# Kernel tuning notes

Hardware: AMD Instinct MI355X
Metric: run time of the kernel (lower is better)

## Reference

```python
import jax, jax.numpy as jnp
import numpy as np

FILTER = 3
STRIDE = 1


def setup_inputs() -> dict:
    key = jax.random.key(0)
    ks = jax.random.split(key, 6)
    B, P, N, d_in, d_ein, d_model = 16, 4, 4096, 128, 32, 128
    e_dim = FILTER * (FILTER - 1) * d_ein  # 192
    adj = jax.random.uniform(ks[0], (N, N), jnp.float32)
    features = jax.random.normal(ks[1], (B, N, d_in), jnp.float32)
    edge_features = jax.random.normal(ks[2], (B, N, e_dim), jnp.float32)
    mask = jax.random.uniform(ks[3], (P, N, 1), jnp.float32)
    W = jax.random.normal(ks[4], (FILTER * d_in + e_dim, d_model), jnp.float32) * 0.02
    b = jnp.zeros((d_model,), jnp.float32)
    return dict(adj=adj, features=features, edge_features=edge_features, mask=mask, W=W, b=b)


def reference(adj, features, edge_features, mask, W, b):
    Fs, S = FILTER, STRIDE
    B, N, d_in = features.shape
    # padding rule from _padding(): below_pad = filter - (N % stride or stride)
    below_pad = N % S
    below_pad = S if below_pad == 0 else below_pad
    below_pad = Fs - below_pad  # = 2 for stride=1, filter=3
    n_out = (N + below_pad - Fs) // S + 1  # = N

    feat_pad = jnp.pad(features, ((0, 0), (0, below_pad), (0, 0)))
    idx = jnp.arange(n_out)[:, None] * S + jnp.arange(Fs)[None, :]  # [n_out, F]
    win = feat_pad[:, idx, :]  # [B, n_out, F, d_in] (gather = torch unfold windows)
    jump = win.mean(axis=2)    # features.unfold(...).sum(-1)/filter -> [B, n_out, d_in]
    # torch unfold puts filter dim last: [B, n_out, d_in, F]; flatten(-2,-1) is d_in-major
    feat_flat = jnp.swapaxes(win, -1, -2).reshape(B, n_out, Fs * d_in)

    mask_pad = jnp.pad(mask, ((0, 0), (0, below_pad), (0, 0)))
    m = mask_pad[:, idx, :].max(axis=2)  # [P, n_out, 1]

    feat_cat = jnp.concatenate([feat_flat, edge_features], axis=-1)  # [B, n_out, 576]
    out = jax.nn.relu(feat_cat @ W + b)  # dropout is identity in eval
    res = out + jump  # residual (res=True)

    P = m.shape[0]
    d_model = out.shape[-1]
    out_m = (m * out.reshape(-1, P, n_out, d_model)).reshape(-1, n_out, d_model)
    res_m = (m * res.reshape(-1, P, n_out, d_model)).reshape(-1, n_out, d_model)
    return adj, res_m, out_m, m
```

## Files before the change

kernel.cpp:

```cpp
#include <hip/hip_runtime.h>
#include <hip/hip_bf16.h>

typedef __attribute__((ext_vector_type(8))) short short8;
typedef __attribute__((ext_vector_type(4))) float floatx4;

#define NN     4096
#define DIN    128
#define EDIM   192
#define DMODEL 128

__device__ __forceinline__ unsigned short f2bf(float f) {
    union { float f; unsigned int i; } x; x.f = f;
    unsigned int u = x.i;
    u += 0x7FFFu + ((u >> 16) & 1u);
    return (unsigned short)(u >> 16);
}

__device__ __forceinline__ unsigned int pk2(float lo, float hi) {
    union { __hip_bfloat162 v; unsigned int u; } cv;
    cv.v = __float22bfloat162_rn(make_float2(lo, hi));
    return cv.u;
}

__device__ __forceinline__ short8 cvt8(const float4 a, const float4 b) {
    union { short8 s; unsigned int u[4]; } r;
    r.u[0] = pk2(a.x, a.y);
    r.u[1] = pk2(a.z, a.w);
    r.u[2] = pk2(b.x, b.y);
    r.u[3] = pk2(b.z, b.w);
    return r.s;
}

__global__ void prep_w(const float* __restrict__ W, unsigned short* __restrict__ wf) {
    const int t = blockIdx.x * 256 + threadIdx.x;
    const int jj   = t & 7;
    const int lane = (t >> 3) & 63;
    const int ct   = (t >> 9) & 7;
    const int gs   = t >> 12;
    const int kt = gs * 32 + ((lane >> 4) << 3) + jj;
    const int korig = (kt < 384) ? ((kt & 127) * 3 + (kt >> 7)) : kt;
    const int n = ct * 16 + (lane & 15);
    wf[t] = f2bf(W[korig * DMODEL + n]);
}

__global__ __launch_bounds__(256, 2) void main_k(
    const float* __restrict__ feat,
    const float* __restrict__ edgef,
    const unsigned short* __restrict__ wfrag,
    const float* __restrict__ bias,
    const float* __restrict__ mask,
    const floatx4* __restrict__ adj4,
    floatx4* __restrict__ o_adj4,
    float* __restrict__ o_res,
    float* __restrict__ o_out,
    float* __restrict__ o_m)
{
    __shared__ float m3s[128];

    const int tid  = threadIdx.x;
    const int lane = tid & 63;
    const int wv   = tid >> 6;
    const int nn   = lane & 15;
    const int quad = lane >> 4;

    const int blk = blockIdx.x;
    const int b   = blk >> 5;
    const int i0  = (blk & 31) << 7;
    const int p   = b & 3;

    if (tid < 128) {
        const int i = i0 + tid;
        float v = mask[p * NN + i];
        if (i + 1 < NN) v = fmaxf(v, mask[p * NN + i + 1]);
        if (i + 2 < NN) v = fmaxf(v, mask[p * NN + i + 2]);
        m3s[tid] = v;
        if (b < 4) o_m[p * NN + i] = v;
    }
    __syncthreads();

    const float* fb = feat  + (size_t)b * NN * DIN;
    const float* eb = edgef + (size_t)b * NN * EDIM;

    const int rowb = i0 + wv * 32 + nn;

    floatx4 acc[2][8];
    #pragma unroll
    for (int rt = 0; rt < 2; ++rt)
        #pragma unroll
        for (int ct = 0; ct < 8; ++ct)
            acc[rt][ct] = (floatx4){0.f, 0.f, 0.f, 0.f};

    const short8* wf8 = (const short8*)wfrag;

    #pragma unroll
    for (int j = 0; j < 3; ++j) {
        #pragma unroll
        for (int sl = 0; sl < 4; ++sl) {
            const int gs = j * 4 + sl;
            short8 bfr[8];
            #pragma unroll
            for (int ct = 0; ct < 8; ++ct)
                bfr[ct] = wf8[(gs * 8 + ct) * 64 + lane];
            short8 afr[2];
            #pragma unroll
            for (int rt = 0; rt < 2; ++rt) {
                const int row = rowb + rt * 16 + j;
                float4 a0 = make_float4(0.f, 0.f, 0.f, 0.f);
                float4 a1 = a0;
                if (row < NN) {
                    const float* s = fb + (size_t)row * DIN + sl * 32 + quad * 8;
                    a0 = *(const float4*)s;
                    a1 = *(const float4*)(s + 4);
                }
                afr[rt] = cvt8(a0, a1);
            }
            #pragma unroll
            for (int rt = 0; rt < 2; ++rt)
                #pragma unroll
                for (int ct = 0; ct < 8; ++ct)
                    acc[rt][ct] = __builtin_amdgcn_mfma_f32_16x16x32_bf16(
                        afr[rt], bfr[ct], acc[rt][ct], 0, 0, 0);
        }
    }

    #pragma unroll
    for (int eg = 0; eg < 6; ++eg) {
        const int gs = 12 + eg;
        short8 bfr[8];
        #pragma unroll
        for (int ct = 0; ct < 8; ++ct)
            bfr[ct] = wf8[(gs * 8 + ct) * 64 + lane];
        short8 afr[2];
        #pragma unroll
        for (int rt = 0; rt < 2; ++rt) {
            const int row = rowb + rt * 16;
            const float* s = eb + (size_t)row * EDIM + eg * 32 + quad * 8;
            const float4 a0 = *(const float4*)s;
            const float4 a1 = *(const float4*)(s + 4);
            afr[rt] = cvt8(a0, a1);
        }
        #pragma unroll
        for (int rt = 0; rt < 2; ++rt)
            #pragma unroll
            for (int ct = 0; ct < 8; ++ct)
                acc[rt][ct] = __builtin_amdgcn_mfma_f32_16x16x32_bf16(
                    afr[rt], bfr[ct], acc[rt][ct], 0, 0, 0);
    }

    float biasv[8];
    #pragma unroll
    for (int ct = 0; ct < 8; ++ct)
        biasv[ct] = bias[ct * 16 + nn];

    const float inv3 = 1.0f / 3.0f;

    #pragma unroll
    for (int rt = 0; rt < 2; ++rt) {
        const int rbase = wv * 32 + rt * 16 + quad * 4;
        float mv[4];
        #pragma unroll
        for (int reg = 0; reg < 4; ++reg)
            mv[reg] = m3s[rbase + reg];
        #pragma unroll
        for (int ct = 0; ct < 8; ++ct) {
            const int col = ct * 16 + nn;
            float fv[6];
            #pragma unroll
            for (int t6 = 0; t6 < 6; ++t6) {
                const int row = i0 + rbase + t6;
                fv[t6] = (row < NN) ? fb[(size_t)row * DIN + col] : 0.f;
            }
            #pragma unroll
            for (int reg = 0; reg < 4; ++reg) {
                float o = acc[rt][ct][reg] + biasv[ct];
                o = fmaxf(o, 0.f);
                const float jmp = (fv[reg] + fv[reg + 1] + fv[reg + 2]) * inv3;
                const size_t off = ((size_t)b * NN + (i0 + rbase + reg)) * DMODEL + col;
                const float mm = mv[reg];
                __builtin_nontemporal_store(mm * o, &o_out[off]);
                __builtin_nontemporal_store(mm * (o + jmp), &o_res[off]);
            }
        }
    }

    {
        const int idx = blk * 256 + tid;
        #pragma unroll
        for (int i = 0; i < 32; ++i) {
            const floatx4 v = __builtin_nontemporal_load(&adj4[idx + i * 131072]);
            __builtin_nontemporal_store(v, &o_adj4[idx + i * 131072]);
        }
    }
}

extern "C" void kernel_launch(void* const* d_in, const int* in_sizes, int n_in,
                              void* d_out, int out_size, void* d_ws, size_t ws_size,
                              hipStream_t stream) {
    const float* adj   = (const float*)d_in[0];
    const float* feat  = (const float*)d_in[1];
    const float* edgef = (const float*)d_in[2];
    const float* mask  = (const float*)d_in[3];
    const float* W     = (const float*)d_in[4];
    const float* bias  = (const float*)d_in[5];

    float* out   = (float*)d_out;
    float* o_adj = out;
    float* o_res = out + (size_t)16777216;
    float* o_out = o_res + (size_t)8388608;
    float* o_m   = o_out + (size_t)8388608;

    unsigned short* wfrag = (unsigned short*)d_ws;

    prep_w<<<288, 256, 0, stream>>>(W, wfrag);
    main_k<<<512, 256, 0, stream>>>(feat, edgef, wfrag, bias, mask,
                                    (const floatx4*)adj, (floatx4*)o_adj,
                                    o_res, o_out, o_m);
}
```

Measured before the change: 273.8 us.

## Halve rows per block and double grid for higher occupancy

Each block now processes 64 rows instead of 128, with one 16-row MFMA tile per wave instead of two. The grid doubles to 1024 blocks and launch bounds allow four blocks per CU, halving accumulator registers. The aim is more waves in flight to hide memory latency in this bandwidth-bound kernel. The trade-off is that weight fragments are loaded twice as often per output row, and the adj copy per block is halved.

```diff
diff --git a/kernel.cpp b/kernel.cpp
--- a/kernel.cpp
+++ b/kernel.cpp
@@ -43,7 +43,7 @@
     wf[t] = f2bf(W[korig * DMODEL + n]);
 }
 
-__global__ __launch_bounds__(256, 2) void main_k(
+__global__ __launch_bounds__(256, 4) void main_k(
     const float* __restrict__ feat,
     const float* __restrict__ edgef,
     const unsigned short* __restrict__ wfrag,
@@ -55,7 +55,7 @@
     float* __restrict__ o_out,
     float* __restrict__ o_m)
 {
-    __shared__ float m3s[128];
+    __shared__ float m3s[64];
 
     const int tid  = threadIdx.x;
     const int lane = tid & 63;
@@ -64,11 +64,11 @@
     const int quad = lane >> 4;
 
     const int blk = blockIdx.x;
-    const int b   = blk >> 5;
-    const int i0  = (blk & 31) << 7;
+    const int b   = blk >> 6;
+    const int i0  = (blk & 63) << 6;
     const int p   = b & 3;
 
-    if (tid < 128) {
+    if (tid < 64) {
         const int i = i0 + tid;
         float v = mask[p * NN + i];
         if (i + 1 < NN) v = fmaxf(v, mask[p * NN + i + 1]);
@@ -81,14 +81,12 @@
     const float* fb = feat  + (size_t)b * NN * DIN;
     const float* eb = edgef + (size_t)b * NN * EDIM;
 
-    const int rowb = i0 + wv * 32 + nn;
-
-    floatx4 acc[2][8];
-    #pragma unroll
-    for (int rt = 0; rt < 2; ++rt)
-        #pragma unroll
-        for (int ct = 0; ct < 8; ++ct)
-            acc[rt][ct] = (floatx4){0.f, 0.f, 0.f, 0.f};
+    const int rowb = i0 + wv * 16 + nn;
+
+    floatx4 acc[8];
+    #pragma unroll
+    for (int ct = 0; ct < 8; ++ct)
+        acc[ct] = (floatx4){0.f, 0.f, 0.f, 0.f};
 
     const short8* wf8 = (const short8*)wfrag;
 
@@ -101,25 +99,19 @@
             #pragma unroll
             for (int ct = 0; ct < 8; ++ct)
                 bfr[ct] = wf8[(gs * 8 + ct) * 64 + lane];
-            short8 afr[2];
+            const int row = rowb + j;
+            float4 a0 = make_float4(0.f, 0.f, 0.f, 0.f);
+            float4 a1 = a0;
+            if (row < NN) {
+                const float* s = fb + (size_t)row * DIN + sl * 32 + quad * 8;
+                a0 = *(const float4*)s;
+                a1 = *(const float4*)(s + 4);
+            }
+            const short8 afr = cvt8(a0, a1);
             #pragma unroll
-            for (int rt = 0; rt < 2; ++rt) {
-                const int row = rowb + rt * 16 + j;
-                float4 a0 = make_float4(0.f, 0.f, 0.f, 0.f);
-                float4 a1 = a0;
-                if (row < NN) {
-                    const float* s = fb + (size_t)row * DIN + sl * 32 + quad * 8;
-                    a0 = *(const float4*)s;
-                    a1 = *(const float4*)(s + 4);
-                }
-                afr[rt] = cvt8(a0, a1);
-            }
-            #pragma unroll
-            for (int rt = 0; rt < 2; ++rt)
-                #pragma unroll
-                for (int ct = 0; ct < 8; ++ct)
-                    acc[rt][ct] = __builtin_amdgcn_mfma_f32_16x16x32_bf16(
-                        afr[rt], bfr[ct], acc[rt][ct], 0, 0, 0);
+            for (int ct = 0; ct < 8; ++ct)
+                acc[ct] = __builtin_amdgcn_mfma_f32_16x16x32_bf16(
+                    afr, bfr[ct], acc[ct], 0, 0, 0);
         }
     }
 
@@ -130,21 +122,14 @@
         #pragma unroll
         for (int ct = 0; ct < 8; ++ct)
             bfr[ct] = wf8[(gs * 8 + ct) * 64 + lane];
-        short8 afr[2];
-        #pragma unroll
-        for (int rt = 0; rt < 2; ++rt) {
-            const int row = rowb + rt * 16;
-            const float* s = eb + (size_t)row * EDIM + eg * 32 + quad * 8;
-            const float4 a0 = *(const float4*)s;
-            const float4 a1 = *(const float4*)(s + 4);
-            afr[rt] = cvt8(a0, a1);
-        }
-        #pragma unroll
-        for (int rt = 0; rt < 2; ++rt)
-            #pragma unroll
-            for (int ct = 0; ct < 8; ++ct)
-                acc[rt][ct] = __builtin_amdgcn_mfma_f32_16x16x32_bf16(
-                    afr[rt], bfr[ct], acc[rt][ct], 0, 0, 0);
+        const float* s = eb + (size_t)rowb * EDIM + eg * 32 + quad * 8;
+        const float4 a0 = *(const float4*)s;
+        const float4 a1 = *(const float4*)(s + 4);
+        const short8 afr = cvt8(a0, a1);
+        #pragma unroll
+        for (int ct = 0; ct < 8; ++ct)
+            acc[ct] = __builtin_amdgcn_mfma_f32_16x16x32_bf16(
+                afr, bfr[ct], acc[ct], 0, 0, 0);
     }
 
     float biasv[8];
@@ -153,42 +138,39 @@
         biasv[ct] = bias[ct * 16 + nn];
 
     const float inv3 = 1.0f / 3.0f;
-
-    #pragma unroll
-    for (int rt = 0; rt < 2; ++rt) {
-        const int rbase = wv * 32 + rt * 16 + quad * 4;
-        float mv[4];
-        #pragma unroll
-        for (int reg = 0; reg < 4; ++reg)
-            mv[reg] = m3s[rbase + reg];
-        #pragma unroll
-        for (int ct = 0; ct < 8; ++ct) {
-            const int col = ct * 16 + nn;
-            float fv[6];
-            #pragma unroll
-            for (int t6 = 0; t6 < 6; ++t6) {
-                const int row = i0 + rbase + t6;
-                fv[t6] = (row < NN) ? fb[(size_t)row * DIN + col] : 0.f;
-            }
-            #pragma unroll
-            for (int reg = 0; reg < 4; ++reg) {
-                float o = acc[rt][ct][reg] + biasv[ct];
-                o = fmaxf(o, 0.f);
-                const float jmp = (fv[reg] + fv[reg + 1] + fv[reg + 2]) * inv3;
-                const size_t off = ((size_t)b * NN + (i0 + rbase + reg)) * DMODEL + col;
-                const float mm = mv[reg];
-                __builtin_nontemporal_store(mm * o, &o_out[off]);
-                __builtin_nontemporal_store(mm * (o + jmp), &o_res[off]);
-            }
+    const int rbase = wv * 16 + quad * 4;
+    float mv[4];
+    #pragma unroll
+    for (int reg = 0; reg < 4; ++reg)
+        mv[reg] = m3s[rbase + reg];
+
+    #pragma unroll
+    for (int ct = 0; ct < 8; ++ct) {
+        const int col = ct * 16 + nn;
+        float fv[6];
+        #pragma unroll
+        for (int t6 = 0; t6 < 6; ++t6) {
+            const int row = i0 + rbase + t6;
+            fv[t6] = (row < NN) ? fb[(size_t)row * DIN + col] : 0.f;
+        }
+        #pragma unroll
+        for (int reg = 0; reg < 4; ++reg) {
+            float o = acc[ct][reg] + biasv[ct];
+            o = fmaxf(o, 0.f);
+            const float jmp = (fv[reg] + fv[reg + 1] + fv[reg + 2]) * inv3;
+            const size_t off = ((size_t)b * NN + (i0 + rbase + reg)) * DMODEL + col;
+            const float mm = mv[reg];
+            __builtin_nontemporal_store(mm * o, &o_out[off]);
+            __builtin_nontemporal_store(mm * (o + jmp), &o_res[off]);
         }
     }
 
     {
         const int idx = blk * 256 + tid;
         #pragma unroll
-        for (int i = 0; i < 32; ++i) {
-            const floatx4 v = __builtin_nontemporal_load(&adj4[idx + i * 131072]);
-            __builtin_nontemporal_store(v, &o_adj4[idx + i * 131072]);
+        for (int i = 0; i < 16; ++i) {
+            const floatx4 v = __builtin_nontemporal_load(&adj4[idx + i * 262144]);
+            __builtin_nontemporal_store(v, &o_adj4[idx + i * 262144]);
         }
     }
 }
@@ -212,7 +194,7 @@
     unsigned short* wfrag = (unsigned short*)d_ws;
 
     prep_w<<<288, 256, 0, stream>>>(W, wfrag);
-    main_k<<<512, 256, 0, stream>>>(feat, edgef, wfrag, bias, mask,
-                                    (const floatx4*)adj, (floatx4*)o_adj,
-                                    o_res, o_out, o_m);
-}
+    main_k<<<1024, 256, 0, stream>>>(feat, edgef, wfrag, bias, mask,
+                                     (const floatx4*)adj, (floatx4*)o_adj,
+                                     o_res, o_out, o_m);
+}
```

Result: slower. 284.4 us (+3.9%).

## Stage weight fragments through double-buffered LDS via direct global-to-LDS loads

Applied to the files above, without the earlier changes.

Weight fragments are no longer loaded from global memory into registers by every wave. Each K-step's 8 KB weight slab is now cooperatively copied into a double-buffered LDS area with global_load_lds, while the next step's activation rows are prefetched into registers. This removes the redundant per-wave weight traffic and overlaps loads with MFMA work. The cost is one block-wide barrier per step and 16 KB of extra LDS, which may reduce occupancy. The kernel is probably bound by the large adj copy and output stores, so the GEMM part matters less.

```diff
diff --git a/kernel.cpp b/kernel.cpp
--- a/kernel.cpp
+++ b/kernel.cpp
@@ -29,6 +29,13 @@
     r.u[2] = pk2(b.x, b.y);
     r.u[3] = pk2(b.z, b.w);
     return r.s;
+}
+
+__device__ __forceinline__ void gl_lds16(const void* g, void* l) {
+    __builtin_amdgcn_global_load_lds(
+        (const __attribute__((address_space(1))) unsigned int*)g,
+        (__attribute__((address_space(3))) unsigned int*)l,
+        16, 0, 0);
 }
 
 __global__ void prep_w(const float* __restrict__ W, unsigned short* __restrict__ wf) {
@@ -55,6 +62,7 @@
     float* __restrict__ o_out,
     float* __restrict__ o_m)
 {
+    __shared__ __align__(16) char lbuf[2][8192];
     __shared__ float m3s[128];
 
     const int tid  = threadIdx.x;
@@ -67,6 +75,10 @@
     const int b   = blk >> 5;
     const int i0  = (blk & 31) << 7;
     const int p   = b & 3;
+
+    const float* fb = feat  + (size_t)b * NN * DIN;
+    const float* eb = edgef + (size_t)b * NN * EDIM;
+    const int rowb = i0 + wv * 32 + nn;
 
     if (tid < 128) {
         const int i = i0 + tid;
@@ -76,12 +88,43 @@
         m3s[tid] = v;
         if (b < 4) o_m[p * NN + i] = v;
     }
-    __syncthreads();
-
-    const float* fb = feat  + (size_t)b * NN * DIN;
-    const float* eb = edgef + (size_t)b * NN * EDIM;
-
-    const int rowb = i0 + wv * 32 + nn;
+
+    const char* wsrc = (const char*)wfrag;
+
+    auto stageB = [&](int s, int bi) {
+        const char* src = wsrc + s * 8192 + wv * 2048 + lane * 16;
+        char* dst = &lbuf[bi][wv * 2048];
+        gl_lds16(src, dst);
+        gl_lds16(src + 1024, dst + 1024);
+    };
+
+    const float4 zf4 = make_float4(0.f, 0.f, 0.f, 0.f);
+
+    auto loadA = [&](int s, float4& a00, float4& a01, float4& a10, float4& a11) {
+        if (s < 12) {
+            const int j = s >> 2, sl = s & 3;
+            const int off = sl * 32 + quad * 8;
+            const int r0 = rowb + j;
+            a00 = zf4; a01 = zf4;
+            if (r0 < NN) {
+                const float* sp = fb + (size_t)r0 * DIN + off;
+                a00 = *(const float4*)sp; a01 = *(const float4*)(sp + 4);
+            }
+            const int r1 = rowb + 16 + j;
+            a10 = zf4; a11 = zf4;
+            if (r1 < NN) {
+                const float* sp = fb + (size_t)r1 * DIN + off;
+                a10 = *(const float4*)sp; a11 = *(const float4*)(sp + 4);
+            }
+        } else {
+            const int eg = s - 12;
+            const int off = eg * 32 + quad * 8;
+            const float* sp0 = eb + (size_t)rowb * EDIM + off;
+            a00 = *(const float4*)sp0; a01 = *(const float4*)(sp0 + 4);
+            const float* sp1 = eb + (size_t)(rowb + 16) * EDIM + off;
+            a10 = *(const float4*)sp1; a11 = *(const float4*)(sp1 + 4);
+        }
+    };
 
     floatx4 acc[2][8];
     #pragma unroll
@@ -90,61 +133,29 @@
         for (int ct = 0; ct < 8; ++ct)
             acc[rt][ct] = (floatx4){0.f, 0.f, 0.f, 0.f};
 
-    const short8* wf8 = (const short8*)wfrag;
-
-    #pragma unroll
-    for (int j = 0; j < 3; ++j) {
-        #pragma unroll
-        for (int sl = 0; sl < 4; ++sl) {
-            const int gs = j * 4 + sl;
-            short8 bfr[8];
-            #pragma unroll
-            for (int ct = 0; ct < 8; ++ct)
-                bfr[ct] = wf8[(gs * 8 + ct) * 64 + lane];
-            short8 afr[2];
-            #pragma unroll
-            for (int rt = 0; rt < 2; ++rt) {
-                const int row = rowb + rt * 16 + j;
-                float4 a0 = make_float4(0.f, 0.f, 0.f, 0.f);
-                float4 a1 = a0;
-                if (row < NN) {
-                    const float* s = fb + (size_t)row * DIN + sl * 32 + quad * 8;
-                    a0 = *(const float4*)s;
-                    a1 = *(const float4*)(s + 4);
-                }
-                afr[rt] = cvt8(a0, a1);
-            }
-            #pragma unroll
-            for (int rt = 0; rt < 2; ++rt)
-                #pragma unroll
-                for (int ct = 0; ct < 8; ++ct)
-                    acc[rt][ct] = __builtin_amdgcn_mfma_f32_16x16x32_bf16(
-                        afr[rt], bfr[ct], acc[rt][ct], 0, 0, 0);
-        }
-    }
-
-    #pragma unroll
-    for (int eg = 0; eg < 6; ++eg) {
-        const int gs = 12 + eg;
-        short8 bfr[8];
-        #pragma unroll
-        for (int ct = 0; ct < 8; ++ct)
-            bfr[ct] = wf8[(gs * 8 + ct) * 64 + lane];
-        short8 afr[2];
-        #pragma unroll
-        for (int rt = 0; rt < 2; ++rt) {
-            const int row = rowb + rt * 16;
-            const float* s = eb + (size_t)row * EDIM + eg * 32 + quad * 8;
-            const float4 a0 = *(const float4*)s;
-            const float4 a1 = *(const float4*)(s + 4);
-            afr[rt] = cvt8(a0, a1);
-        }
-        #pragma unroll
-        for (int rt = 0; rt < 2; ++rt)
-            #pragma unroll
-            for (int ct = 0; ct < 8; ++ct)
-                acc[rt][ct] = __builtin_amdgcn_mfma_f32_16x16x32_bf16(
-                    afr[rt], bfr[ct], acc[rt][ct], 0, 0, 0);
+    float4 a00, a01, a10, a11, n00, n01, n10, n11;
+    stageB(0, 0);
+    loadA(0, a00, a01, a10, a11);
+    __syncthreads();
+
+    #pragma unroll
+    for (int s = 0; s < 18; ++s) {
+        const int cur = s & 1;
+        if (s < 17) {
+            stageB(s + 1, cur ^ 1);
+            loadA(s + 1, n00, n01, n10, n11);
+        }
+        const short8* bl = (const short8*)(&lbuf[cur][0]);
+        const short8 af0 = cvt8(a00, a01);
+        const short8 af1 = cvt8(a10, a11);
+        #pragma unroll
+        for (int ct = 0; ct < 8; ++ct) {
+            const short8 bfr = bl[ct * 64 + lane];
+            acc[0][ct] = __builtin_amdgcn_mfma_f32_16x16x32_bf16(af0, bfr, acc[0][ct], 0, 0, 0);
+            acc[1][ct] = __builtin_amdgcn_mfma_f32_16x16x32_bf16(af1, bfr, acc[1][ct], 0, 0, 0);
+        }
+        a00 = n00; a01 = n01; a10 = n10; a11 = n11;
+        __syncthreads();
     }
 
     float biasv[8];
```

After: 272.6 us. Within noise of the previous version (-0.4%).
